# Optimization experiments

Hardware: AMD Instinct MI355X
Metric: run time of the kernel (lower is better)

Reference implementation:

```python
import jax, jax.numpy as jnp
import numpy as np

TOPK = 8

def setup_inputs() -> dict:
    key = jax.random.key(0)
    k1, k2, k3, k4 = jax.random.split(key, 4)
    B, T, D = 4, 4096, 1024
    SUB, HALF, VDIM = 512, D // 2, 128
    query = jax.random.normal(k1, (B, T, D), dtype=jnp.float32)
    codebook1 = jax.random.normal(k2, (SUB, HALF), dtype=jnp.float32) * 0.02
    codebook2 = jax.random.normal(k3, (SUB, HALF), dtype=jnp.float32) * 0.02
    values = jax.random.normal(k4, (SUB * SUB, VDIM), dtype=jnp.float32) * 0.02
    return {"query": query, "codebook1": codebook1, "codebook2": codebook2, "values": values}

def reference(query, codebook1, codebook2, values):
    B, T, D = query.shape
    sub_keys, half = codebook1.shape
    q1 = query[..., :half]
    q2 = query[..., half:2 * half]
    # [B,T,sub_keys] score matrices
    s1 = jnp.einsum('btd,kd->btk', q1, codebook1)
    s2 = jnp.einsum('btd,kd->btk', q2, codebook2)
    tk1_vals, tk1_idx = jax.lax.top_k(s1, TOPK)
    tk2_vals, tk2_idx = jax.lax.top_k(s2, TOPK)
    # cartesian combine: [B,T,TOPK,TOPK] -> [B,T,TOPK*TOPK]
    full_idx = (tk1_idx[..., :, None] * sub_keys + tk2_idx[..., None, :]).reshape(B, T, -1)
    w1 = jax.nn.softmax(tk1_vals, axis=-1)
    w2 = jax.nn.softmax(tk2_vals, axis=-1)
    weights = (w1[..., :, None] * w2[..., None, :]).reshape(B, T, -1)
    vals = values[full_idx]  # [B,T,TOPK^2,value_dim] gather
    return jnp.einsum('btk,btkv->btv', weights, vals)
```

## Files before the change

kernel.cpp:

```cpp
#include <hip/hip_runtime.h>
#include <hip/hip_bf16.h>
#include <math.h>

#define NTOK 16384
#define DDIM 1024
#define HALF 512
#define SUB  512
#define KDIM 512
#define TOPK 8
#define NCAND 16
#define VDIM 128
#define TMB 32

typedef __attribute__((ext_vector_type(8))) short bf16x8;
typedef __attribute__((ext_vector_type(4))) float f32x4;

static __device__ __forceinline__ unsigned short f2bf(float x) {
    union { float f; unsigned u; } v; v.f = x;
    unsigned r = v.u + 0x7FFF + ((v.u >> 16) & 1);
    return (unsigned short)(r >> 16);
}

static __device__ __forceinline__ void split_bf(float x, unsigned short& h, unsigned short& l) {
    h = f2bf(x);
    union { unsigned u; float f; } hv; hv.u = ((unsigned)h) << 16;
    l = f2bf(x - hv.f);
}

__global__ __launch_bounds__(256)
void cvt_bfrag(const float* __restrict__ cb1, const float* __restrict__ cb2,
               unsigned short* __restrict__ Bh, unsigned short* __restrict__ Bl)
{
    int fid  = blockIdx.x * 256 + threadIdx.x;
    int lane = fid & 63;
    int kc   = (fid >> 6) & 15;
    int nt   = (fid >> 10) & 15;
    int chh  = (fid >> 14) & 3;
    const float* cb = (chh >> 1) ? cb2 : cb1;
    int n  = (chh & 1) * 256 + nt * 16 + (lane & 15);
    int kb = kc * 32 + (lane >> 4) * 8;
    const float* src = cb + (size_t)n * KDIM + kb;
    float4 f0 = *(const float4*)src;
    float4 f1 = *(const float4*)(src + 4);
    unsigned short hh[8], ll[8];
    split_bf(f0.x, hh[0], ll[0]); split_bf(f0.y, hh[1], ll[1]);
    split_bf(f0.z, hh[2], ll[2]); split_bf(f0.w, hh[3], ll[3]);
    split_bf(f1.x, hh[4], ll[4]); split_bf(f1.y, hh[5], ll[5]);
    split_bf(f1.z, hh[6], ll[6]); split_bf(f1.w, hh[7], ll[7]);
    *(int4*)(Bh + (size_t)fid * 8) = *(const int4*)hh;
    *(int4*)(Bl + (size_t)fid * 8) = *(const int4*)ll;
}

__global__ __launch_bounds__(256, 2)
void score_topk_mfma(const float* __restrict__ query,
                     const float* __restrict__ cb1f,
                     const float* __restrict__ cb2f,
                     const unsigned short* __restrict__ Bh,
                     const unsigned short* __restrict__ Bl,
                     int*   __restrict__ tk_idx,
                     float* __restrict__ tk_val)
{
    __shared__ char smem[65536];
    char* sAh = smem;
    char* sAl = smem + 32768;
    float* sS = (float*)smem;

    const int tid  = threadIdx.x;
    const int hf   = blockIdx.y;
    const int tok0 = blockIdx.x * TMB;
    const float* __restrict__ cbf = hf ? cb2f : cb1f;
    const int qoff = hf * HALF;

    const int lane = tid & 63;
    const int wid  = tid >> 6;
    const int tokg = wid >> 1;
    const int chf  = wid & 1;
    const int l15  = lane & 15;
    const int lh   = lane >> 4;
    const int l7   = lane & 7;

    #pragma unroll
    for (int i = 0; i < 8; i++) {
        int c   = i * 256 + tid;
        int row = c >> 6;
        int b8  = c & 63;
        const float* src = query + (size_t)(tok0 + row) * DDIM + qoff + b8 * 8;
        float4 f0 = *(const float4*)(src);
        float4 f1 = *(const float4*)(src + 4);
        unsigned short hh[8], ll[8];
        split_bf(f0.x, hh[0], ll[0]); split_bf(f0.y, hh[1], ll[1]);
        split_bf(f0.z, hh[2], ll[2]); split_bf(f0.w, hh[3], ll[3]);
        split_bf(f1.x, hh[4], ll[4]); split_bf(f1.y, hh[5], ll[5]);
        split_bf(f1.z, hh[6], ll[6]); split_bf(f1.w, hh[7], ll[7]);
        int boff = row * 1024 + ((b8 * 16) ^ ((row & 7) << 4));
        *(int4*)(sAh + boff) = *(const int4*)hh;
        *(int4*)(sAl + boff) = *(const int4*)ll;
    }
    __syncthreads();

    bf16x8 ah[16], al[16];
    #pragma unroll
    for (int kc = 0; kc < 16; kc++) {
        int aoff = (tokg * 16 + l15) * 1024 + ((kc * 64 + lh * 16) ^ (l7 << 4));
        ah[kc] = *(const bf16x8*)(sAh + aoff);
        al[kc] = *(const bf16x8*)(sAl + aoff);
    }
    __syncthreads();

    const char* bhp = (const char*)Bh + (size_t)(hf * 2 + chf) * 262144 + lane * 16;
    const char* blp = (const char*)Bl + (size_t)(hf * 2 + chf) * 262144 + lane * 16;
    int4 rh[8], rl[8];
    #pragma unroll
    for (int p = 0; p < 8; p++) {
        rh[p] = *(const int4*)(bhp + p * 1024);
        rl[p] = *(const int4*)(blp + p * 1024);
    }

    for (int nt = 0; nt < 16; nt++) {
        f32x4 aX = {0.f,0.f,0.f,0.f}, aY = {0.f,0.f,0.f,0.f}, aZ = {0.f,0.f,0.f,0.f};
        #pragma unroll
        for (int kc = 0; kc < 16; kc++) {
            const int s = nt * 16 + kc;
            const int slot = kc & 7;
            union { int4 i; bf16x8 b; } ubh, ubl;
            ubh.i = rh[slot]; ubl.i = rl[slot];
            rh[slot] = *(const int4*)(bhp + ((s + 8) & 255) * 1024);
            rl[slot] = *(const int4*)(blp + ((s + 8) & 255) * 1024);
            aX = __builtin_amdgcn_mfma_f32_16x16x32_bf16(ah[kc], ubh.b, aX, 0, 0, 0);
            aY = __builtin_amdgcn_mfma_f32_16x16x32_bf16(al[kc], ubh.b, aY, 0, 0, 0);
            aZ = __builtin_amdgcn_mfma_f32_16x16x32_bf16(ah[kc], ubl.b, aZ, 0, 0, 0);
        }
        f32x4 sc = aX + aY + aZ;
        #pragma unroll
        for (int r = 0; r < 4; r++) {
            int t = tokg * 16 + lh * 4 + r;
            int c = chf * 256 + nt * 16 + l15;
            sS[t * SUB + (c ^ (lh << 3))] = sc[r];
        }
    }
    __syncthreads();

    for (int v = 0; v < 8; v++) {
        const int t   = wid * 8 + v;
        const int tok = tok0 + t;
        const int hsh = ((t >> 2) & 3) << 3;

        float sv[8];
        #pragma unroll
        for (int j = 0; j < 8; j++) sv[j] = sS[t * SUB + ((lane + 64 * j) ^ hsh)];

        float m = sv[0];
        #pragma unroll
        for (int j = 1; j < 8; j++) m = fmaxf(m, sv[j]);
        #pragma unroll
        for (int off = 32; off > 0; off >>= 1) m = fmaxf(m, __shfl_xor(m, off));

        auto wave_cnt = [&](float tau) -> int {
            int c = 0;
            #pragma unroll
            for (int j = 0; j < 8; j++)
                c += __popcll(__ballot(sv[j] > tau));
            return c;
        };

        float lo = m - 3.0f, hi = m;
        while (wave_cnt(lo) < 9) lo -= 3.0f;
        for (int it = 0; it < 17; it++) {
            float mid = 0.5f * (lo + hi);
            if (wave_cnt(mid) >= 9) lo = mid; else hi = mid;
        }
        int ch8 = wave_cnt(hi);

        float v8 = 1e30f, v9 = -1e30f;
        #pragma unroll
        for (int j = 0; j < 8; j++) {
            bool sel = sv[j] > hi;
            v8 = sel ? fminf(v8, sv[j]) : v8;
            v9 = sel ? v9 : fmaxf(v9, sv[j]);
        }
        #pragma unroll
        for (int off = 32; off > 0; off >>= 1) {
            v8 = fminf(v8, __shfl_xor(v8, off));
            v9 = fmaxf(v9, __shfl_xor(v9, off));
        }

        if (ch8 == 8 && (v8 - v9) > 6e-5f) {
            int base = 0;
            #pragma unroll
            for (int j = 0; j < 8; j++) {
                unsigned long long mk = __ballot(sv[j] > hi);
                if (sv[j] > hi) {
                    int pos = base + __popcll(mk & ((1ULL << lane) - 1ULL));
                    tk_idx[((size_t)tok * 2 + hf) * TOPK + pos] = lane + 64 * j;
                    tk_val[((size_t)tok * 2 + hf) * TOPK + pos] = sv[j];
                }
                base += __popcll(mk);
            }
        } else {
            int cand[NCAND];
            #pragma unroll
            for (int r = 0; r < NCAND; r++) {
                float bv = sv[0]; int bj = 0;
                #pragma unroll
                for (int j = 1; j < 8; j++) if (sv[j] > bv) { bv = sv[j]; bj = j; }
                int bidx = lane + 64 * bj;
                #pragma unroll
                for (int off = 32; off > 0; off >>= 1) {
                    float ov = __shfl_xor(bv, off);
                    int   oi = __shfl_xor(bidx, off);
                    if (ov > bv || (ov == bv && oi < bidx)) { bv = ov; bidx = oi; }
                }
                cand[r] = bidx;
                int jj = bidx >> 6;
                if ((bidx & 63) == lane) {
                    #pragma unroll
                    for (int j = 0; j < 8; j++) if (j == jj) sv[j] = -INFINITY;
                }
            }
            double qd[8];
            #pragma unroll
            for (int j = 0; j < 8; j++)
                qd[j] = (double)query[(size_t)tok * DDIM + qoff + lane + 64 * j];
            double rv[NCAND];
            #pragma unroll
            for (int r = 0; r < NCAND; r++) {
                const float* __restrict__ crow = &cbf[(size_t)cand[r] * KDIM];
                double a = 0.0;
                #pragma unroll
                for (int j = 0; j < 8; j++)
                    a = fma(qd[j], (double)crow[lane + 64 * j], a);
                #pragma unroll
                for (int off = 32; off > 0; off >>= 1)
                    a += __shfl_xor(a, off);
                rv[r] = a;
            }
            if (lane == 0) {
                #pragma unroll
                for (int r = 0; r < NCAND; r++) {
                    int rk = 0;
                    #pragma unroll
                    for (int mm = 0; mm < NCAND; mm++)
                        if (rv[mm] > rv[r] || (rv[mm] == rv[r] && cand[mm] < cand[r])) rk++;
                    if (rk < TOPK) {
                        tk_idx[((size_t)tok * 2 + hf) * TOPK + rk] = cand[r];
                        tk_val[((size_t)tok * 2 + hf) * TOPK + rk] = (float)rv[r];
                    }
                }
            }
        }
    }
}

__global__ __launch_bounds__(256)
void gather_kernel(const float* __restrict__ values,
                   const int*   __restrict__ tk_idx,
                   const float* __restrict__ tk_val,
                   float* __restrict__ out)
{
    const int tid  = threadIdx.x;
    const int lane = tid & 63;
    const int tok  = blockIdx.x * 4 + (tid >> 6);

    const int b1 = (tok * 2 + 0) * TOPK;
    const int b2 = (tok * 2 + 1) * TOPK;

    float v1[8], v2[8]; int i1[8], i2[8];
    #pragma unroll
    for (int j = 0; j < 8; j++) {
        i1[j] = tk_idx[b1 + j]; v1[j] = tk_val[b1 + j];
        i2[j] = tk_idx[b2 + j]; v2[j] = tk_val[b2 + j];
    }

    float m1 = v1[0], m2 = v2[0];
    #pragma unroll
    for (int j = 1; j < 8; j++) { m1 = fmaxf(m1, v1[j]); m2 = fmaxf(m2, v2[j]); }

    float w1[8], w2[8], s1 = 0.f, s2 = 0.f;
    #pragma unroll
    for (int j = 0; j < 8; j++) {
        w1[j] = expf(v1[j] - m1); s1 += w1[j];
        w2[j] = expf(v2[j] - m2); s2 += w2[j];
    }
    const float inv1 = 1.f / s1, inv2 = 1.f / s2;
    #pragma unroll
    for (int j = 0; j < 8; j++) { w1[j] *= inv1; w2[j] *= inv2; }

    float2 acc = make_float2(0.f, 0.f);
    #pragma unroll
    for (int i = 0; i < 8; i++) {
        const int rb = i1[i] * SUB;
        const float wi = w1[i];
        #pragma unroll
        for (int j = 0; j < 8; j++) {
            const float w = wi * w2[j];
            const float* __restrict__ row = values + (size_t)(rb + i2[j]) * VDIM;
            float2 tv = *(const float2*)&row[lane * 2];
            acc.x = fmaf(w, tv.x, acc.x);
            acc.y = fmaf(w, tv.y, acc.y);
        }
    }
    *(float2*)&out[(size_t)tok * VDIM + lane * 2] = acc;
}

extern "C" void kernel_launch(void* const* d_in, const int* in_sizes, int n_in,
                              void* d_out, int out_size, void* d_ws, size_t ws_size,
                              hipStream_t stream) {
    const float* query  = (const float*)d_in[0];
    const float* cb1    = (const float*)d_in[1];
    const float* cb2    = (const float*)d_in[2];
    const float* values = (const float*)d_in[3];
    float* out = (float*)d_out;

    char* ws = (char*)d_ws;
    int*            tk_idx = (int*)ws;
    float*          tk_val = (float*)(ws + (1u << 20));
    unsigned short* Bh     = (unsigned short*)(ws + (2u << 20));
    unsigned short* Bl     = (unsigned short*)(ws + (3u << 20));

    cvt_bfrag<<<256, 256, 0, stream>>>(cb1, cb2, Bh, Bl);
    dim3 g1(NTOK / TMB, 2);
    score_topk_mfma<<<g1, 256, 0, stream>>>(query, cb1, cb2, Bh, Bl, tk_idx, tk_val);
    gather_kernel<<<NTOK / 4, 256, 0, stream>>>(values, tk_idx, tk_val, out);
}
```

Baseline: 228.5 us.

## Halve token tile, give each wave 128 columns, and loop kc outermost

Shrinks the token tile from 32 to 16 so the kernel uses half the shared memory and can target 4 blocks per CU instead of 2. Each wave now covers a 128-column slice with 8 accumulators in a kc-outer loop, reading A fragments from LDS per kc instead of holding all 16 in registers. The B-fragment packing kernel is reordered to match. The top-k bisection starts from a tighter 0.5 window with fewer iterations, which could lose precision or need more expansion steps.

Measured after the change: 215.5 us. 5.7% less time.

```diff
diff --git a/kernel.cpp b/kernel.cpp
--- a/kernel.cpp
+++ b/kernel.cpp
@@ -10,7 +10,7 @@
 #define TOPK 8
 #define NCAND 16
 #define VDIM 128
-#define TMB 32
+#define TMB 16
 
 typedef __attribute__((ext_vector_type(8))) short bf16x8;
 typedef __attribute__((ext_vector_type(4))) float f32x4;
@@ -33,11 +33,12 @@
 {
     int fid  = blockIdx.x * 256 + threadIdx.x;
     int lane = fid & 63;
-    int kc   = (fid >> 6) & 15;
-    int nt   = (fid >> 10) & 15;
-    int chh  = (fid >> 14) & 3;
-    const float* cb = (chh >> 1) ? cb2 : cb1;
-    int n  = (chh & 1) * 256 + nt * 16 + (lane & 15);
+    int nt   = (fid >> 6) & 7;
+    int kc   = (fid >> 9) & 15;
+    int cq   = (fid >> 13) & 3;
+    int hf   = (fid >> 15) & 1;
+    const float* cb = hf ? cb2 : cb1;
+    int n  = cq * 128 + nt * 16 + (lane & 15);
     int kb = kc * 32 + (lane >> 4) * 8;
     const float* src = cb + (size_t)n * KDIM + kb;
     float4 f0 = *(const float4*)src;
@@ -51,7 +52,7 @@
     *(int4*)(Bl + (size_t)fid * 8) = *(const int4*)ll;
 }
 
-__global__ __launch_bounds__(256, 2)
+__global__ __launch_bounds__(256, 4)
 void score_topk_mfma(const float* __restrict__ query,
                      const float* __restrict__ cb1f,
                      const float* __restrict__ cb2f,
@@ -60,9 +61,9 @@
                      int*   __restrict__ tk_idx,
                      float* __restrict__ tk_val)
 {
-    __shared__ char smem[65536];
+    __shared__ char smem[32768];
     char* sAh = smem;
-    char* sAl = smem + 32768;
+    char* sAl = smem + 16384;
     float* sS = (float*)smem;
 
     const int tid  = threadIdx.x;
@@ -73,14 +74,12 @@
 
     const int lane = tid & 63;
     const int wid  = tid >> 6;
-    const int tokg = wid >> 1;
-    const int chf  = wid & 1;
     const int l15  = lane & 15;
     const int lh   = lane >> 4;
     const int l7   = lane & 7;
 
     #pragma unroll
-    for (int i = 0; i < 8; i++) {
+    for (int i = 0; i < 4; i++) {
         int c   = i * 256 + tid;
         int row = c >> 6;
         int b8  = c & 63;
@@ -98,50 +97,51 @@
     }
     __syncthreads();
 
-    bf16x8 ah[16], al[16];
-    #pragma unroll
-    for (int kc = 0; kc < 16; kc++) {
-        int aoff = (tokg * 16 + l15) * 1024 + ((kc * 64 + lh * 16) ^ (l7 << 4));
-        ah[kc] = *(const bf16x8*)(sAh + aoff);
-        al[kc] = *(const bf16x8*)(sAl + aoff);
-    }
-    __syncthreads();
-
-    const char* bhp = (const char*)Bh + (size_t)(hf * 2 + chf) * 262144 + lane * 16;
-    const char* blp = (const char*)Bl + (size_t)(hf * 2 + chf) * 262144 + lane * 16;
-    int4 rh[8], rl[8];
-    #pragma unroll
-    for (int p = 0; p < 8; p++) {
+    const char* bhp = (const char*)Bh + (size_t)(hf * 4 + wid) * 131072 + lane * 16;
+    const char* blp = (const char*)Bl + (size_t)(hf * 4 + wid) * 131072 + lane * 16;
+
+    int4 rh[4], rl[4];
+    #pragma unroll
+    for (int p = 0; p < 4; p++) {
         rh[p] = *(const int4*)(bhp + p * 1024);
         rl[p] = *(const int4*)(blp + p * 1024);
     }
 
-    for (int nt = 0; nt < 16; nt++) {
-        f32x4 aX = {0.f,0.f,0.f,0.f}, aY = {0.f,0.f,0.f,0.f}, aZ = {0.f,0.f,0.f,0.f};
-        #pragma unroll
-        for (int kc = 0; kc < 16; kc++) {
-            const int s = nt * 16 + kc;
-            const int slot = kc & 7;
+    f32x4 acc[8];
+    #pragma unroll
+    for (int nt = 0; nt < 8; nt++) acc[nt] = (f32x4){0.f, 0.f, 0.f, 0.f};
+
+    for (int kc = 0; kc < 16; kc++) {
+        const int aoff = l15 * 1024 + ((kc * 64 + lh * 16) ^ (l7 << 4));
+        const bf16x8 ah = *(const bf16x8*)(sAh + aoff);
+        const bf16x8 al = *(const bf16x8*)(sAl + aoff);
+        #pragma unroll
+        for (int nt = 0; nt < 8; nt++) {
+            const int slot = nt & 3;
             union { int4 i; bf16x8 b; } ubh, ubl;
             ubh.i = rh[slot]; ubl.i = rl[slot];
-            rh[slot] = *(const int4*)(bhp + ((s + 8) & 255) * 1024);
-            rl[slot] = *(const int4*)(blp + ((s + 8) & 255) * 1024);
-            aX = __builtin_amdgcn_mfma_f32_16x16x32_bf16(ah[kc], ubh.b, aX, 0, 0, 0);
-            aY = __builtin_amdgcn_mfma_f32_16x16x32_bf16(al[kc], ubh.b, aY, 0, 0, 0);
-            aZ = __builtin_amdgcn_mfma_f32_16x16x32_bf16(ah[kc], ubl.b, aZ, 0, 0, 0);
-        }
-        f32x4 sc = aX + aY + aZ;
+            const int sp = (kc * 8 + nt + 4) & 127;
+            rh[slot] = *(const int4*)(bhp + sp * 1024);
+            rl[slot] = *(const int4*)(blp + sp * 1024);
+            acc[nt] = __builtin_amdgcn_mfma_f32_16x16x32_bf16(ah, ubh.b, acc[nt], 0, 0, 0);
+            acc[nt] = __builtin_amdgcn_mfma_f32_16x16x32_bf16(al, ubh.b, acc[nt], 0, 0, 0);
+            acc[nt] = __builtin_amdgcn_mfma_f32_16x16x32_bf16(ah, ubl.b, acc[nt], 0, 0, 0);
+        }
+    }
+    __syncthreads();
+
+    #pragma unroll
+    for (int nt = 0; nt < 8; nt++)
         #pragma unroll
         for (int r = 0; r < 4; r++) {
-            int t = tokg * 16 + lh * 4 + r;
-            int c = chf * 256 + nt * 16 + l15;
-            sS[t * SUB + (c ^ (lh << 3))] = sc[r];
-        }
-    }
+            int t = lh * 4 + r;
+            int c = wid * 128 + nt * 16 + l15;
+            sS[t * SUB + (c ^ (lh << 3))] = acc[nt][r];
+        }
     __syncthreads();
 
-    for (int v = 0; v < 8; v++) {
-        const int t   = wid * 8 + v;
+    for (int v = 0; v < 4; v++) {
+        const int t   = wid * 4 + v;
         const int tok = tok0 + t;
         const int hsh = ((t >> 2) & 3) << 3;
 
@@ -163,9 +163,9 @@
             return c;
         };
 
-        float lo = m - 3.0f, hi = m;
-        while (wave_cnt(lo) < 9) lo -= 3.0f;
-        for (int it = 0; it < 17; it++) {
+        float lo = m - 0.5f, hi = m;
+        while (wave_cnt(lo) < 9) lo -= 0.5f;
+        for (int it = 0; it < 14; it++) {
             float mid = 0.5f * (lo + hi);
             if (wave_cnt(mid) >= 9) lo = mid; else hi = mid;
         }
```
